# Optimization experiments

Hardware: AMD Instinct MI355X
Metric: run time of the kernel (lower is better)

The kernel has to match this reference:

```python
import jax, jax.numpy as jnp
import numpy as np

B, C, H, W = 8, 128, 64, 64


def setup_inputs() -> dict:
    key = jax.random.key(0)
    ks = jax.random.split(key, 8)
    s = 1.0 / np.sqrt(C)
    return {
        "x1": jax.random.normal(ks[0], (B, C, H, W), dtype=jnp.float32),
        "x2": jax.random.normal(ks[1], (B, C, H, W), dtype=jnp.float32),
        "Wq": jax.random.normal(ks[2], (C, C), dtype=jnp.float32) * s,
        "bq": jax.random.normal(ks[3], (C,), dtype=jnp.float32) * s,
        "Wk": jax.random.normal(ks[4], (C, C), dtype=jnp.float32) * s,
        "bk": jax.random.normal(ks[5], (C,), dtype=jnp.float32) * s,
        "Wv": jax.random.normal(ks[6], (C, C), dtype=jnp.float32) * s,
        "bv": jax.random.normal(ks[7], (C,), dtype=jnp.float32) * s,
    }


def reference(x1, x2, Wq, bq, Wk, bk, Wv, bv):
    b, c, h, w = x1.shape
    n = h * w
    # 1x1 conv == channel matmul per pixel; flatten spatial dims -> [b, c, n]
    x1f = x1.reshape(b, c, n)
    x2f = x2.reshape(b, c, n)
    q = jnp.einsum("oc,bcn->bno", Wq, x1f) + bq[None, None, :]  # [b, n, c]
    k = jnp.einsum("oc,bcn->bon", Wk, x2f) + bk[None, :, None]  # [b, c, n]
    v = jnp.einsum("oc,bcn->bon", Wv, x2f) + bv[None, :, None]  # [b, c, n]
    energy = jnp.einsum("bnc,bcm->bnm", q, k)                   # [b, n, n] (unscaled)
    attention = jax.nn.softmax(energy, axis=-1)
    # out[b,c,i] = sum_j v[b,c,j] * attention[b,i,j]
    out = jnp.einsum("bcj,bij->bci", v, attention)
    return out.reshape(b, c, h, w)
```

## Files before the change

kernel.cpp:

```cpp
#include <hip/hip_runtime.h>

typedef float f4 __attribute__((ext_vector_type(4)));
typedef float f16v __attribute__((ext_vector_type(16)));
typedef _Float16 hf;
typedef __fp16 fp16x2 __attribute__((ext_vector_type(2)));
typedef hf h8 __attribute__((ext_vector_type(8)));
typedef unsigned short ushort_t;
typedef unsigned int uint_t;
typedef uint_t u4 __attribute__((ext_vector_type(4)));

#define BATCH 8
#define CH 128
#define NPIX 4096
#define LOG2E 1.4426950408889634f
#define XSTR 65
#define RESCALE_THR 8.0f

__device__ inline f16v mfma32h(h8 a, h8 b, f16v c) {
    return __builtin_amdgcn_mfma_f32_32x32x16_f16(a, b, c, 0, 0, 0);
}

__device__ inline uint_t pk2h(float a, float b) {
    fp16x2 pp = __builtin_amdgcn_cvt_pkrtz(a, b);
    union { fp16x2 v; uint_t u; } cv;
    cv.v = pp;
    return cv.u;
}

__device__ inline void pl32swap(uint_t& a, uint_t& b) {
    asm("v_permlane32_swap_b32 %0, %1" : "+v"(a), "+v"(b));
}

typedef __attribute__((address_space(3))) uint_t lds_uint;
typedef __attribute__((address_space(1))) const uint_t global_uint;
__device__ inline void dma16(const void* g, void* l) {
    __builtin_amdgcn_global_load_lds((global_uint*)g, (lds_uint*)l, 16, 0, 0);
}

__global__ __launch_bounds__(256) void wprep_kernel(const float* __restrict__ Wq,
                                                    const float* __restrict__ Wk,
                                                    const float* __restrict__ Wv,
                                                    hf* __restrict__ WqT, hf* __restrict__ WkT,
                                                    hf* __restrict__ Wv16) {
    int m = blockIdx.x;
    const float* W = (m == 0) ? Wq : (m == 1) ? Wk : Wv;
    float s = (m == 0) ? LOG2E : 1.0f;
    for (int idx = threadIdx.x; idx < CH * CH; idx += 256) {
        int o = idx >> 7, c = idx & 127;
        float v = W[idx] * s;
        if (m == 0) WqT[c * CH + o] = (hf)v;
        else if (m == 1) WkT[c * CH + o] = (hf)v;
        else Wv16[idx] = (hf)v;
    }
}

__global__ __launch_bounds__(256) void qkv_kernel(const float* __restrict__ x1,
                                                  const float* __restrict__ x2,
                                                  const hf* __restrict__ WqT,
                                                  const hf* __restrict__ WkT,
                                                  const hf* __restrict__ Wv16,
                                                  const float* __restrict__ bq,
                                                  const float* __restrict__ bk,
                                                  const float* __restrict__ bv,
                                                  hf* __restrict__ Qf, hf* __restrict__ Kf,
                                                  hf* __restrict__ Vf) {
    __shared__ __align__(16) float Xs[CH * XSTR];

    int bid = blockIdx.x;
    int m = bid >> 9;
    int rem = bid & 511;
    int b = rem & 7;
    int n0 = (rem >> 3) << 6;

    const float* X = ((m == 0) ? x1 : x2) + (size_t)b * CH * NPIX;
    const float* bias = (m == 0) ? bq : (m == 1) ? bk : bv;

    int tid = threadIdx.x;
#pragma unroll
    for (int r = 0; r < 8; ++r) {
        int c = 16 * r + (tid >> 4);
        int n4 = (tid & 15) << 2;
        f4 v = *(const f4*)&X[(size_t)c * NPIX + n0 + n4];
#pragma unroll
        for (int j = 0; j < 4; ++j) Xs[c * XSTR + n4 + j] = v[j];
    }
    __syncthreads();

    int lane = tid & 63;
    int w = tid >> 6;
    int h = lane >> 5;
    int m32 = lane & 31;
    int o0 = w * 32;

    h8 wf[8];
    if (m == 2) {
#pragma unroll
        for (int kc = 0; kc < 8; ++kc)
            wf[kc] = *(const h8*)&Wv16[(size_t)(o0 + m32) * CH + kc * 16 + h * 8];
    } else {
        const hf* WT = (m == 0) ? WqT : WkT;
#pragma unroll
        for (int kc = 0; kc < 8; ++kc) {
            h8 t;
#pragma unroll
            for (int j = 0; j < 8; ++j) t[j] = WT[(size_t)(kc * 16 + h * 8 + j) * CH + o0 + m32];
            wf[kc] = t;
        }
    }

    f16v acc[2];
#pragma unroll
    for (int g = 0; g < 2; ++g)
#pragma unroll
        for (int r = 0; r < 16; ++r) acc[g][r] = 0.f;

#pragma unroll
    for (int g = 0; g < 2; ++g) {
        const float* xbase = &Xs[h * 8 * XSTR + g * 32 + m32];
#pragma unroll
        for (int kc = 0; kc < 8; ++kc) {
            h8 xh, xl;
#pragma unroll
            for (int j = 0; j < 8; ++j) {
                float f = xbase[(kc * 16 + j) * XSTR];
                hf hi = (hf)f;
                xh[j] = hi;
                xl[j] = (hf)(f - (float)hi);
            }
            if (m == 2) {
                acc[g] = mfma32h(wf[kc], xh, acc[g]);
                acc[g] = mfma32h(wf[kc], xl, acc[g]);
            } else {
                acc[g] = mfma32h(xh, wf[kc], acc[g]);
                acc[g] = mfma32h(xl, wf[kc], acc[g]);
            }
        }
    }

    if (m < 2) {
        float bval = bias[o0 + m32] * ((m == 0) ? LOG2E : 1.0f);
        hf* Y = ((m == 0) ? Qf : Kf) + (size_t)b * NPIX * CH;
#pragma unroll
        for (int g = 0; g < 2; ++g)
#pragma unroll
            for (int r = 0; r < 16; ++r) {
                int n = n0 + g * 32 + (r & 3) + 8 * (r >> 2) + 4 * h;
                Y[(size_t)n * CH + o0 + m32] = (hf)(acc[g][r] + bval);
            }
    } else {
        hf* Yv = Vf + (size_t)b * CH * NPIX;
#pragma unroll
        for (int g = 0; g < 2; ++g)
#pragma unroll
            for (int r = 0; r < 16; ++r) {
                int o = o0 + (r & 3) + 8 * (r >> 2) + 4 * h;
                Yv[(size_t)o * NPIX + n0 + g * 32 + m32] = (hf)(acc[g][r] + bias[o]);
            }
    }
}

__global__ __launch_bounds__(256, 2) void attn_kernel(const hf* __restrict__ Qf,
                                                      const hf* __restrict__ Kf,
                                                      const hf* __restrict__ Vf,
                                                      hf* __restrict__ Opart,
                                                      float* __restrict__ Mpart,
                                                      float* __restrict__ Lpart) {
    __shared__ __align__(16) ushort_t smem[32768];

    int tid = threadIdx.x;
    int lane = tid & 63;
    int w = tid >> 6;
    int h = lane >> 5;
    int m32 = lane & 31;
    int qh = w >> 1, kh = w & 1;

    int idx = blockIdx.x;
    int b = idx & 7;
    int ks = (idx >> 3) & 1;
    int qt = idx >> 4;
    int i0g = qt << 7;
    int k0g = ks << 11;
    int krow = kh * 32 + m32;

    const hf* Qb = Qf + (size_t)b * NPIX * CH;
    const hf* Kb = Kf + (size_t)b * NPIX * CH;
    const hf* Vb = Vf + (size_t)b * CH * NPIX;

    h8 qf[2][8];
#pragma unroll
    for (int g = 0; g < 2; ++g) {
        size_t row = (size_t)(i0g + qh * 64 + g * 32 + m32) * CH + h * 8;
#pragma unroll
        for (int kc = 0; kc < 8; ++kc) qf[g][kc] = *(const h8*)&Qb[row + kc * 16];
    }

    const hf* pK[4];
    const hf* pV[4];
#pragma unroll
    for (int a = 0; a < 4; ++a) {
        int g = w * 4 + a;
        int rowk = g * 4 + (lane >> 4);
        int lck = (lane & 15) ^ (rowk & 15);
        pK[a] = Kb + (size_t)(k0g + rowk) * CH + lck * 8;
        int rowv = g * 8 + (lane >> 3);
        int lcv = (lane & 7) ^ (rowv & 7);
        pV[a] = Vb + (size_t)rowv * NPIX + k0g + lcv * 8;
    }

#pragma unroll
    for (int a = 0; a < 4; ++a) {
        dma16(pK[a], &smem[(w * 4 + a) * 512]);
        dma16(pV[a], &smem[16384 + (w * 4 + a) * 512]);
        pK[a] += 64 * CH;
        pV[a] += 64;
    }

    f16v accO[2][4];
#pragma unroll
    for (int g = 0; g < 2; ++g)
#pragma unroll
        for (int ct = 0; ct < 4; ++ct)
#pragma unroll
            for (int r = 0; r < 16; ++r) accO[g][ct][r] = 0.f;
    float mprev[2] = {-1e30f, -1e30f};
    float lsum[2] = {0.f, 0.f};

    int pc2s[2];
#pragma unroll
    for (int g2 = 0; g2 < 2; ++g2) pc2s[g2] = (kh * 4 + g2 * 2 + h) ^ (m32 & 7);

    __syncthreads();

    for (int t = 0; t < 32; ++t) {
        int cur = t & 1;
        if (t < 31) {
            int nb = 1 - cur;
#pragma unroll
            for (int a = 0; a < 4; ++a) {
                dma16(pK[a], &smem[nb * 8192 + (w * 4 + a) * 512]);
                dma16(pV[a], &smem[16384 + nb * 8192 + (w * 4 + a) * 512]);
                pK[a] += 64 * CH;
                pV[a] += 64;
            }
        }
        const ushort_t* kb = smem + cur * 8192;
        const ushort_t* vb = smem + 16384 + cur * 8192;

        f16v acc0, acc1;
#pragma unroll
        for (int r = 0; r < 16; ++r) { acc0[r] = 0.f; acc1[r] = 0.f; }
        __builtin_amdgcn_s_setprio(1);
#pragma unroll
        for (int kc = 0; kc < 8; ++kc) {
            int pA = (kc * 2 + h) ^ (m32 & 15);
            h8 ahi = *(const h8*)&kb[krow * 128 + pA * 8];
            acc0 = mfma32h(ahi, qf[0][kc], acc0);
            acc1 = mfma32h(ahi, qf[1][kc], acc1);
        }
        __builtin_amdgcn_s_setprio(0);

        h8 pbp[2][2];
#pragma unroll
        for (int g = 0; g < 2; ++g) {
            f16v& acc = g ? acc1 : acc0;
            float ta = fmaxf(fmaxf(acc[0], acc[1]), acc[2]);
            float tb = fmaxf(fmaxf(acc[3], acc[4]), acc[5]);
            ta = fmaxf(fmaxf(ta, acc[6]), acc[7]);
            tb = fmaxf(fmaxf(tb, acc[8]), acc[9]);
            ta = fmaxf(fmaxf(ta, acc[10]), acc[11]);
            tb = fmaxf(fmaxf(tb, acc[12]), acc[13]);
            ta = fmaxf(fmaxf(ta, acc[14]), acc[15]);
            float tmax = fmaxf(ta, tb);
            tmax = fmaxf(tmax, __shfl_xor(tmax, 32));
            if (__any(tmax > mprev[g] + RESCALE_THR)) {
                float mnew = fmaxf(mprev[g], tmax);
                float alpha = exp2f(mprev[g] - mnew);
                lsum[g] *= alpha;
#pragma unroll
                for (int ct = 0; ct < 4; ++ct)
#pragma unroll
                    for (int r = 0; r < 16; ++r) accO[g][ct][r] *= alpha;
                mprev[g] = mnew;
            }

            float p[16];
#pragma unroll
            for (int r = 0; r < 16; ++r) p[r] = exp2f(acc[r] - mprev[g]);
            float ps[8];
#pragma unroll
            for (int r = 0; r < 8; ++r) ps[r] = p[r] + p[r + 8];
#pragma unroll
            for (int r = 0; r < 4; ++r) ps[r] += ps[r + 4];
            float psum = (ps[0] + ps[1]) + (ps[2] + ps[3]);
            psum += __shfl_xor(psum, 32);
            lsum[g] += psum;

            uint_t pk[8];
#pragma unroll
            for (int t2 = 0; t2 < 8; ++t2) pk[t2] = pk2h(p[2 * t2], p[2 * t2 + 1]);
            pl32swap(pk[0], pk[2]);
            pl32swap(pk[1], pk[3]);
            pl32swap(pk[4], pk[6]);
            pl32swap(pk[5], pk[7]);
#pragma unroll
            for (int g2 = 0; g2 < 2; ++g2) {
                u4 fv;
                fv[0] = pk[g2 * 4 + 0];
                fv[1] = pk[g2 * 4 + 1];
                fv[2] = pk[g2 * 4 + 2];
                fv[3] = pk[g2 * 4 + 3];
                __builtin_memcpy(&pbp[g][g2], &fv, 16);
            }
        }

        __builtin_amdgcn_s_setprio(1);
#pragma unroll
        for (int g2 = 0; g2 < 2; ++g2) {
            int pc2 = pc2s[g2];
#pragma unroll
            for (int ct = 0; ct < 4; ++ct) {
                h8 av = *(const h8*)&vb[(ct * 32 + m32) * 64 + pc2 * 8];
                accO[0][ct] = mfma32h(av, pbp[0][g2], accO[0][ct]);
                accO[1][ct] = mfma32h(av, pbp[1][g2], accO[1][ct]);
            }
        }
        __builtin_amdgcn_s_setprio(0);

        __syncthreads();
    }

    float* scr = (float*)smem;
    if (h == 0) {
#pragma unroll
        for (int g = 0; g < 2; ++g) {
            scr[kh * 128 + qh * 64 + g * 32 + m32] = mprev[g];
            scr[256 + kh * 128 + qh * 64 + g * 32 + m32] = lsum[g];
        }
    }
    __syncthreads();
    float fk[2], Mv[2], Lv[2];
#pragma unroll
    for (int g = 0; g < 2; ++g) {
        float mo = scr[(1 - kh) * 128 + qh * 64 + g * 32 + m32];
        float lo2 = scr[256 + (1 - kh) * 128 + qh * 64 + g * 32 + m32];
        float M = fmaxf(mprev[g], mo);
        fk[g] = exp2f(mprev[g] - M);
        float fo = exp2f(mo - M);
        Mv[g] = M;
        Lv[g] = lsum[g] * fk[g] + lo2 * fo;
    }
    __syncthreads();

    float* mrg = (float*)smem;
    if (kh == 1) {
#pragma unroll
        for (int g = 0; g < 2; ++g)
#pragma unroll
            for (int ct = 0; ct < 4; ++ct)
#pragma unroll
                for (int r = 0; r < 16; ++r) {
                    int ch = ct * 32 + (r & 3) + 8 * (r >> 2) + 4 * h;
                    mrg[ch * 128 + qh * 64 + g * 32 + m32] = accO[g][ct][r] * fk[g];
                }
    }
    __syncthreads();
    if (kh == 0) {
        size_t base = (((size_t)ks * 8 + b) * 32 + qt) * 16384;
        size_t mlb = (((size_t)ks * 8 + b) * 32 + qt) * 128;
#pragma unroll
        for (int g = 0; g < 2; ++g) {
            int q = qh * 64 + g * 32 + m32;
#pragma unroll
            for (int ct = 0; ct < 4; ++ct)
#pragma unroll
                for (int r = 0; r < 16; ++r) {
                    int ch = ct * 32 + (r & 3) + 8 * (r >> 2) + 4 * h;
                    Opart[base + ch * 128 + q] = (hf)(accO[g][ct][r] * fk[g] + mrg[ch * 128 + q]);
                }
            if (h == 0) {
                Mpart[mlb + q] = Mv[g];
                Lpart[mlb + q] = Lv[g];
            }
        }
    }
}

__global__ __launch_bounds__(256) void combine_kernel(const hf* __restrict__ Opart,
                                                      const float* __restrict__ Mp,
                                                      const float* __restrict__ Lp,
                                                      float* __restrict__ out) {
    int idx = blockIdx.x;
    int b = idx & 7;
    int qt = idx >> 3;
    int tid = threadIdx.x;
    int q = tid & 127;
    int ch0 = (tid >> 7) << 6;

    size_t base0 = (((size_t)b) * 32 + qt) * 16384;
    size_t base1 = ((((size_t)8 + b)) * 32 + qt) * 16384;
    size_t ml0 = (((size_t)b) * 32 + qt) * 128 + q;
    size_t ml1 = ((((size_t)8 + b)) * 32 + qt) * 128 + q;

    float M0 = Mp[ml0], M1 = Mp[ml1];
    float L0 = Lp[ml0], L1 = Lp[ml1];
    float M = fmaxf(M0, M1);
    float w0 = exp2f(M0 - M), w1 = exp2f(M1 - M);
    float rd = 1.0f / (w0 * L0 + w1 * L1);

    float* O = out + (size_t)b * CH * NPIX + ((size_t)qt << 7);
#pragma unroll 4
    for (int c = ch0; c < ch0 + 64; ++c) {
        float o0 = (float)Opart[base0 + c * 128 + q];
        float o1 = (float)Opart[base1 + c * 128 + q];
        O[(size_t)c * NPIX + q] = (w0 * o0 + w1 * o1) * rd;
    }
}

extern "C" void kernel_launch(void* const* d_in, const int* in_sizes, int n_in,
                              void* d_out, int out_size, void* d_ws, size_t ws_size,
                              hipStream_t stream) {
    const float* x1 = (const float*)d_in[0];
    const float* x2 = (const float*)d_in[1];
    const float* Wq = (const float*)d_in[2];
    const float* bq = (const float*)d_in[3];
    const float* Wk = (const float*)d_in[4];
    const float* bk = (const float*)d_in[5];
    const float* Wv = (const float*)d_in[6];
    const float* bv = (const float*)d_in[7];
    float* outp = (float*)d_out;

    const size_t N = (size_t)BATCH * NPIX * CH;
    hf* Qf = (hf*)d_ws;
    hf* Kf = Qf + N;
    hf* Vf = Qf + 2 * N;
    hf* WqT = Qf + 3 * N;
    hf* WkT = WqT + CH * CH;
    hf* Wv16 = WqT + 2 * CH * CH;
    hf* Opart = WqT + 3 * CH * CH;
    float* Mp = (float*)(Opart + (size_t)2 * 8 * 32 * 16384);
    float* Lp = Mp + (size_t)2 * 8 * 32 * 128;

    wprep_kernel<<<3, 256, 0, stream>>>(Wq, Wk, Wv, WqT, WkT, Wv16);
    qkv_kernel<<<3 * BATCH * (NPIX / 64), 256, 0, stream>>>(x1, x2, WqT, WkT, Wv16,
                                                            bq, bk, bv, Qf, Kf, Vf);
    attn_kernel<<<BATCH * 2 * (NPIX / 128), 256, 0, stream>>>(Qf, Kf, Vf, Opart, Mp, Lp);
    combine_kernel<<<BATCH * (NPIX / 128), 256, 0, stream>>>(Opart, Mp, Lp, outp);
}
```

Before: 237.1 us.

## Split attention into four key chunks with one query tile per wave

The attention kernel changes from two key splits with a 2x2 wave grid (query half by key half, merged inside the block through LDS) to four key splits where each wave owns 32 queries and walks all keys of its chunk. This drops the in-block merge, halves LDS so three blocks fit per CU, and doubles the grid. The cost is twice the partial-output traffic, handled by a combine kernel that now merges four partials with vectorized loads and stores. The separate weight-prep kernel is also removed: the QKV kernel reads the fp32 weights directly and converts them, saving one launch.

```diff
diff --git a/kernel.cpp b/kernel.cpp
--- a/kernel.cpp
+++ b/kernel.cpp
@@ -37,28 +37,11 @@
     __builtin_amdgcn_global_load_lds((global_uint*)g, (lds_uint*)l, 16, 0, 0);
 }
 
-__global__ __launch_bounds__(256) void wprep_kernel(const float* __restrict__ Wq,
-                                                    const float* __restrict__ Wk,
-                                                    const float* __restrict__ Wv,
-                                                    hf* __restrict__ WqT, hf* __restrict__ WkT,
-                                                    hf* __restrict__ Wv16) {
-    int m = blockIdx.x;
-    const float* W = (m == 0) ? Wq : (m == 1) ? Wk : Wv;
-    float s = (m == 0) ? LOG2E : 1.0f;
-    for (int idx = threadIdx.x; idx < CH * CH; idx += 256) {
-        int o = idx >> 7, c = idx & 127;
-        float v = W[idx] * s;
-        if (m == 0) WqT[c * CH + o] = (hf)v;
-        else if (m == 1) WkT[c * CH + o] = (hf)v;
-        else Wv16[idx] = (hf)v;
-    }
-}
-
 __global__ __launch_bounds__(256) void qkv_kernel(const float* __restrict__ x1,
                                                   const float* __restrict__ x2,
-                                                  const hf* __restrict__ WqT,
-                                                  const hf* __restrict__ WkT,
-                                                  const hf* __restrict__ Wv16,
+                                                  const float* __restrict__ Wq,
+                                                  const float* __restrict__ Wk,
+                                                  const float* __restrict__ Wv,
                                                   const float* __restrict__ bq,
                                                   const float* __restrict__ bk,
                                                   const float* __restrict__ bv,
@@ -92,18 +75,21 @@
     int m32 = lane & 31;
     int o0 = w * 32;
 
+    const float* Wsrc = (m == 0) ? Wq : (m == 1) ? Wk : Wv;
+    float wscale = (m == 0) ? LOG2E : 1.0f;
     h8 wf[8];
-    if (m == 2) {
-#pragma unroll
-        for (int kc = 0; kc < 8; ++kc)
-            wf[kc] = *(const h8*)&Wv16[(size_t)(o0 + m32) * CH + kc * 16 + h * 8];
-    } else {
-        const hf* WT = (m == 0) ? WqT : WkT;
+    {
+        const float* wrow = Wsrc + (size_t)(o0 + m32) * CH;
 #pragma unroll
         for (int kc = 0; kc < 8; ++kc) {
+            f4 a = *(const f4*)&wrow[kc * 16 + h * 8];
+            f4 b2 = *(const f4*)&wrow[kc * 16 + h * 8 + 4];
             h8 t;
 #pragma unroll
-            for (int j = 0; j < 8; ++j) t[j] = WT[(size_t)(kc * 16 + h * 8 + j) * CH + o0 + m32];
+            for (int j = 0; j < 4; ++j) {
+                t[j] = (hf)(a[j] * wscale);
+                t[4 + j] = (hf)(b2[j] * wscale);
+            }
             wf[kc] = t;
         }
     }
@@ -159,75 +145,68 @@
     }
 }
 
-__global__ __launch_bounds__(256, 2) void attn_kernel(const hf* __restrict__ Qf,
+__global__ __launch_bounds__(256, 3) void attn_kernel(const hf* __restrict__ Qf,
                                                       const hf* __restrict__ Kf,
                                                       const hf* __restrict__ Vf,
                                                       hf* __restrict__ Opart,
                                                       float* __restrict__ Mpart,
                                                       float* __restrict__ Lpart) {
-    __shared__ __align__(16) ushort_t smem[32768];
+    __shared__ __align__(16) ushort_t smem[16384];
 
     int tid = threadIdx.x;
     int lane = tid & 63;
     int w = tid >> 6;
     int h = lane >> 5;
     int m32 = lane & 31;
-    int qh = w >> 1, kh = w & 1;
 
     int idx = blockIdx.x;
     int b = idx & 7;
-    int ks = (idx >> 3) & 1;
-    int qt = idx >> 4;
-    int i0g = qt << 7;
-    int k0g = ks << 11;
-    int krow = kh * 32 + m32;
+    int ks = (idx >> 3) & 3;
+    int qt = idx >> 5;
+    int q0 = (qt << 7) + w * 32;
+    int k0g = ks << 10;
 
     const hf* Qb = Qf + (size_t)b * NPIX * CH;
     const hf* Kb = Kf + (size_t)b * NPIX * CH;
     const hf* Vb = Vf + (size_t)b * CH * NPIX;
 
-    h8 qf[2][8];
-#pragma unroll
-    for (int g = 0; g < 2; ++g) {
-        size_t row = (size_t)(i0g + qh * 64 + g * 32 + m32) * CH + h * 8;
-#pragma unroll
-        for (int kc = 0; kc < 8; ++kc) qf[g][kc] = *(const h8*)&Qb[row + kc * 16];
-    }
-
-    const hf* pK[4];
-    const hf* pV[4];
-#pragma unroll
-    for (int a = 0; a < 4; ++a) {
-        int g = w * 4 + a;
-        int rowk = g * 4 + (lane >> 4);
+    h8 qf[8];
+#pragma unroll
+    for (int kc = 0; kc < 8; ++kc)
+        qf[kc] = *(const h8*)&Qb[(size_t)(q0 + m32) * CH + kc * 16 + h * 8];
+
+    const hf* pK[2];
+    const hf* pV[2];
+#pragma unroll
+    for (int a = 0; a < 2; ++a) {
+        int chunk_hi = w * 2 + a;
+        int rowk = chunk_hi * 4 + (lane >> 4);
         int lck = (lane & 15) ^ (rowk & 15);
         pK[a] = Kb + (size_t)(k0g + rowk) * CH + lck * 8;
-        int rowv = g * 8 + (lane >> 3);
-        int lcv = (lane & 7) ^ (rowv & 7);
+        int rowv = chunk_hi * 16 + (lane >> 2);
+        int lcv = (lane & 3) ^ (rowv & 3);
         pV[a] = Vb + (size_t)rowv * NPIX + k0g + lcv * 8;
     }
 
 #pragma unroll
-    for (int a = 0; a < 4; ++a) {
-        dma16(pK[a], &smem[(w * 4 + a) * 512]);
-        dma16(pV[a], &smem[16384 + (w * 4 + a) * 512]);
-        pK[a] += 64 * CH;
-        pV[a] += 64;
-    }
-
-    f16v accO[2][4];
-#pragma unroll
-    for (int g = 0; g < 2; ++g)
-#pragma unroll
-        for (int ct = 0; ct < 4; ++ct)
-#pragma unroll
-            for (int r = 0; r < 16; ++r) accO[g][ct][r] = 0.f;
-    float mprev[2] = {-1e30f, -1e30f};
-    float lsum[2] = {0.f, 0.f};
-
-    int pc2s[2];
-#pragma unroll
-    for (int g2 = 0; g2 < 2; ++g2) pc2s[g2] = (kh * 4 + g2 * 2 + h) ^ (m32 & 7);
+    for (int a = 0; a < 2; ++a) {
+        dma16(pK[a], &smem[(w * 2 + a) * 512]);
+        dma16(pV[a], &smem[8192 + (w * 2 + a) * 512]);
+        pK[a] += 32 * CH;
+        pV[a] += 32;
+    }
+
+    f16v accO[4];
+#pragma unroll
+    for (int ct = 0; ct < 4; ++ct)
+#pragma unroll
+        for (int r = 0; r < 16; ++r) accO[ct][r] = 0.f;
+    float mprev = -1e30f;
+    float lsum = 0.f;
+
+    int pvs[2];
+#pragma unroll
+    for (int g2 = 0; g2 < 2; ++g2) pvs[g2] = (g2 * 2 + h) ^ (m32 & 3);
 
     __syncthreads();
 
@@ -236,92 +215,85 @@
         if (t < 31) {
             int nb = 1 - cur;
 #pragma unroll
-            for (int a = 0; a < 4; ++a) {
-                dma16(pK[a], &smem[nb * 8192 + (w * 4 + a) * 512]);
-                dma16(pV[a], &smem[16384 + nb * 8192 + (w * 4 + a) * 512]);
-                pK[a] += 64 * CH;
-                pV[a] += 64;
-            }
-        }
-        const ushort_t* kb = smem + cur * 8192;
-        const ushort_t* vb = smem + 16384 + cur * 8192;
-
-        f16v acc0, acc1;
-#pragma unroll
-        for (int r = 0; r < 16; ++r) { acc0[r] = 0.f; acc1[r] = 0.f; }
+            for (int a = 0; a < 2; ++a) {
+                dma16(pK[a], &smem[nb * 4096 + (w * 2 + a) * 512]);
+                dma16(pV[a], &smem[8192 + nb * 4096 + (w * 2 + a) * 512]);
+                pK[a] += 32 * CH;
+                pV[a] += 32;
+            }
+        }
+        const ushort_t* kb = smem + cur * 4096;
+        const ushort_t* vb = smem + 8192 + cur * 4096;
+
+        f16v acc;
+#pragma unroll
+        for (int r = 0; r < 16; ++r) acc[r] = 0.f;
         __builtin_amdgcn_s_setprio(1);
 #pragma unroll
         for (int kc = 0; kc < 8; ++kc) {
             int pA = (kc * 2 + h) ^ (m32 & 15);
-            h8 ahi = *(const h8*)&kb[krow * 128 + pA * 8];
-            acc0 = mfma32h(ahi, qf[0][kc], acc0);
-            acc1 = mfma32h(ahi, qf[1][kc], acc1);
+            h8 ahi = *(const h8*)&kb[m32 * 128 + pA * 8];
+            acc = mfma32h(ahi, qf[kc], acc);
         }
         __builtin_amdgcn_s_setprio(0);
 
-        h8 pbp[2][2];
-#pragma unroll
-        for (int g = 0; g < 2; ++g) {
-            f16v& acc = g ? acc1 : acc0;
-            float ta = fmaxf(fmaxf(acc[0], acc[1]), acc[2]);
-            float tb = fmaxf(fmaxf(acc[3], acc[4]), acc[5]);
-            ta = fmaxf(fmaxf(ta, acc[6]), acc[7]);
-            tb = fmaxf(fmaxf(tb, acc[8]), acc[9]);
-            ta = fmaxf(fmaxf(ta, acc[10]), acc[11]);
-            tb = fmaxf(fmaxf(tb, acc[12]), acc[13]);
-            ta = fmaxf(fmaxf(ta, acc[14]), acc[15]);
-            float tmax = fmaxf(ta, tb);
-            tmax = fmaxf(tmax, __shfl_xor(tmax, 32));
-            if (__any(tmax > mprev[g] + RESCALE_THR)) {
-                float mnew = fmaxf(mprev[g], tmax);
-                float alpha = exp2f(mprev[g] - mnew);
-                lsum[g] *= alpha;
-#pragma unroll
-                for (int ct = 0; ct < 4; ++ct)
-#pragma unroll
-                    for (int r = 0; r < 16; ++r) accO[g][ct][r] *= alpha;
-                mprev[g] = mnew;
-            }
-
-            float p[16];
-#pragma unroll
-            for (int r = 0; r < 16; ++r) p[r] = exp2f(acc[r] - mprev[g]);
-            float ps[8];
-#pragma unroll
-            for (int r = 0; r < 8; ++r) ps[r] = p[r] + p[r + 8];
-#pragma unroll
-            for (int r = 0; r < 4; ++r) ps[r] += ps[r + 4];
-            float psum = (ps[0] + ps[1]) + (ps[2] + ps[3]);
-            psum += __shfl_xor(psum, 32);
-            lsum[g] += psum;
-
-            uint_t pk[8];
-#pragma unroll
-            for (int t2 = 0; t2 < 8; ++t2) pk[t2] = pk2h(p[2 * t2], p[2 * t2 + 1]);
-            pl32swap(pk[0], pk[2]);
-            pl32swap(pk[1], pk[3]);
-            pl32swap(pk[4], pk[6]);
-            pl32swap(pk[5], pk[7]);
-#pragma unroll
-            for (int g2 = 0; g2 < 2; ++g2) {
-                u4 fv;
-                fv[0] = pk[g2 * 4 + 0];
-                fv[1] = pk[g2 * 4 + 1];
-                fv[2] = pk[g2 * 4 + 2];
-                fv[3] = pk[g2 * 4 + 3];
-                __builtin_memcpy(&pbp[g][g2], &fv, 16);
-            }
+        float ta = fmaxf(fmaxf(acc[0], acc[1]), acc[2]);
+        float tb = fmaxf(fmaxf(acc[3], acc[4]), acc[5]);
+        ta = fmaxf(fmaxf(ta, acc[6]), acc[7]);
+        tb = fmaxf(fmaxf(tb, acc[8]), acc[9]);
+        ta = fmaxf(fmaxf(ta, acc[10]), acc[11]);
+        tb = fmaxf(fmaxf(tb, acc[12]), acc[13]);
+        ta = fmaxf(fmaxf(ta, acc[14]), acc[15]);
+        float tmax = fmaxf(ta, tb);
+        tmax = fmaxf(tmax, __shfl_xor(tmax, 32));
+        if (__any(tmax > mprev + RESCALE_THR)) {
+            float mnew = fmaxf(mprev, tmax);
+            float alpha = exp2f(mprev - mnew);
+            lsum *= alpha;
+#pragma unroll
+            for (int ct = 0; ct < 4; ++ct)
+#pragma unroll
+                for (int r = 0; r < 16; ++r) accO[ct][r] *= alpha;
+            mprev = mnew;
+        }
+
+        uint_t pk[8];
+        float ps0 = 0.f, ps1 = 0.f;
+#pragma unroll
+        for (int t2 = 0; t2 < 8; ++t2) {
+            float e0 = exp2f(acc[2 * t2] - mprev);
+            float e1 = exp2f(acc[2 * t2 + 1] - mprev);
+            ps0 += e0;
+            ps1 += e1;
+            pk[t2] = pk2h(e0, e1);
+        }
+        float psum = ps0 + ps1;
+        psum += __shfl_xor(psum, 32);
+        lsum += psum;
+
+        pl32swap(pk[0], pk[2]);
+        pl32swap(pk[1], pk[3]);
+        pl32swap(pk[4], pk[6]);
+        pl32swap(pk[5], pk[7]);
+        h8 pbp[2];
+#pragma unroll
+        for (int g2 = 0; g2 < 2; ++g2) {
+            u4 fv;
+            fv[0] = pk[g2 * 4 + 0];
+            fv[1] = pk[g2 * 4 + 1];
+            fv[2] = pk[g2 * 4 + 2];
+            fv[3] = pk[g2 * 4 + 3];
+            __builtin_memcpy(&pbp[g2], &fv, 16);
         }
 
         __builtin_amdgcn_s_setprio(1);
 #pragma unroll
         for (int g2 = 0; g2 < 2; ++g2) {
-            int pc2 = pc2s[g2];
+            int pv = pvs[g2];
 #pragma unroll
             for (int ct = 0; ct < 4; ++ct) {
-                h8 av = *(const h8*)&vb[(ct * 32 + m32) * 64 + pc2 * 8];
-                accO[0][ct] = mfma32h(av, pbp[0][g2], accO[0][ct]);
-                accO[1][ct] = mfma32h(av, pbp[1][g2], accO[1][ct]);
+                h8 av = *(const h8*)&vb[(ct * 32 + m32) * 32 + pv * 8];
+                accO[ct] = mfma32h(av, pbp[g2], accO[ct]);
             }
         }
         __builtin_amdgcn_s_setprio(0);
@@ -329,59 +301,19 @@
         __syncthreads();
     }
 
-    float* scr = (float*)smem;
+    size_t base = (((size_t)ks * 8 + b) * 32 + qt) * 16384;
+    size_t mlb = (((size_t)ks * 8 + b) * 32 + qt) * 128;
+    int q = w * 32 + m32;
+#pragma unroll
+    for (int ct = 0; ct < 4; ++ct)
+#pragma unroll
+        for (int r = 0; r < 16; ++r) {
+            int ch = ct * 32 + (r & 3) + 8 * (r >> 2) + 4 * h;
+            Opart[base + ch * 128 + q] = (hf)accO[ct][r];
+        }
     if (h == 0) {
-#pragma unroll
-        for (int g = 0; g < 2; ++g) {
-            scr[kh * 128 + qh * 64 + g * 32 + m32] = mprev[g];
-            scr[256 + kh * 128 + qh * 64 + g * 32 + m32] = lsum[g];
-        }
-    }
-    __syncthreads();
-    float fk[2], Mv[2], Lv[2];
-#pragma unroll
-    for (int g = 0; g < 2; ++g) {
-        float mo = scr[(1 - kh) * 128 + qh * 64 + g * 32 + m32];
-        float lo2 = scr[256 + (1 - kh) * 128 + qh * 64 + g * 32 + m32];
-        float M = fmaxf(mprev[g], mo);
-        fk[g] = exp2f(mprev[g] - M);
-        float fo = exp2f(mo - M);
-        Mv[g] = M;
-        Lv[g] = lsum[g] * fk[g] + lo2 * fo;
-    }
-    __syncthreads();
-
-    float* mrg = (float*)smem;
-    if (kh == 1) {
-#pragma unroll
-        for (int g = 0; g < 2; ++g)
-#pragma unroll
-            for (int ct = 0; ct < 4; ++ct)
-#pragma unroll
-                for (int r = 0; r < 16; ++r) {
-                    int ch = ct * 32 + (r & 3) + 8 * (r >> 2) + 4 * h;
-                    mrg[ch * 128 + qh * 64 + g * 32 + m32] = accO[g][ct][r] * fk[g];
-                }
-    }
-    __syncthreads();
-    if (kh == 0) {
-        size_t base = (((size_t)ks * 8 + b) * 32 + qt) * 16384;
-        size_t mlb = (((size_t)ks * 8 + b) * 32 + qt) * 128;
-#pragma unroll
-        for (int g = 0; g < 2; ++g) {
-            int q = qh * 64 + g * 32 + m32;
-#pragma unroll
-            for (int ct = 0; ct < 4; ++ct)
-#pragma unroll
-                for (int r = 0; r < 16; ++r) {
-                    int ch = ct * 32 + (r & 3) + 8 * (r >> 2) + 4 * h;
-                    Opart[base + ch * 128 + q] = (hf)(accO[g][ct][r] * fk[g] + mrg[ch * 128 + q]);
-                }
-            if (h == 0) {
-                Mpart[mlb + q] = Mv[g];
-                Lpart[mlb + q] = Lv[g];
-            }
-        }
+        Mpart[mlb + q] = mprev;
+        Lpart[mlb + q] = lsum;
     }
 }
 
@@ -390,29 +322,72 @@
                                                       const float* __restrict__ Lp,
                                                       float* __restrict__ out) {
     int idx = blockIdx.x;
-    int b = idx & 7;
-    int qt = idx >> 3;
+    int chh = idx & 1;
+    int b = (idx >> 1) & 7;
+    int qt = idx >> 4;
     int tid = threadIdx.x;
-    int q = tid & 127;
-    int ch0 = (tid >> 7) << 6;
-
-    size_t base0 = (((size_t)b) * 32 + qt) * 16384;
-    size_t base1 = ((((size_t)8 + b)) * 32 + qt) * 16384;
-    size_t ml0 = (((size_t)b) * 32 + qt) * 128 + q;
-    size_t ml1 = ((((size_t)8 + b)) * 32 + qt) * 128 + q;
-
-    float M0 = Mp[ml0], M1 = Mp[ml1];
-    float L0 = Lp[ml0], L1 = Lp[ml1];
-    float M = fmaxf(M0, M1);
-    float w0 = exp2f(M0 - M), w1 = exp2f(M1 - M);
-    float rd = 1.0f / (w0 * L0 + w1 * L1);
-
-    float* O = out + (size_t)b * CH * NPIX + ((size_t)qt << 7);
-#pragma unroll 4
-    for (int c = ch0; c < ch0 + 64; ++c) {
-        float o0 = (float)Opart[base0 + c * 128 + q];
-        float o1 = (float)Opart[base1 + c * 128 + q];
-        O[(size_t)c * NPIX + q] = (w0 * o0 + w1 * o1) * rd;
+    int q8 = (tid & 15) << 3;
+    int chl = tid >> 4;
+
+    size_t tile = (size_t)b * 32 + qt;
+
+    float Marr[4][8], Larr[4][8];
+#pragma unroll
+    for (int p = 0; p < 4; ++p) {
+        const float* mp_ = Mp + ((size_t)p * 256 + tile) * 128 + q8;
+        const float* lp_ = Lp + ((size_t)p * 256 + tile) * 128 + q8;
+        f4 ma = *(const f4*)mp_;
+        f4 mb = *(const f4*)(mp_ + 4);
+        f4 la = *(const f4*)lp_;
+        f4 lb = *(const f4*)(lp_ + 4);
+#pragma unroll
+        for (int j = 0; j < 4; ++j) {
+            Marr[p][j] = ma[j];
+            Marr[p][4 + j] = mb[j];
+            Larr[p][j] = la[j];
+            Larr[p][4 + j] = lb[j];
+        }
+    }
+
+    float wgt[4][8];
+#pragma unroll
+    for (int j = 0; j < 8; ++j) {
+        float M = fmaxf(fmaxf(Marr[0][j], Marr[1][j]), fmaxf(Marr[2][j], Marr[3][j]));
+        float L = 0.f;
+#pragma unroll
+        for (int p = 0; p < 4; ++p) {
+            float w_ = exp2f(Marr[p][j] - M);
+            wgt[p][j] = w_;
+            L += w_ * Larr[p][j];
+        }
+        float rd = 1.0f / L;
+#pragma unroll
+        for (int p = 0; p < 4; ++p) wgt[p][j] *= rd;
+    }
+
+    const hf* ob[4];
+#pragma unroll
+    for (int p = 0; p < 4; ++p) ob[p] = Opart + ((size_t)p * 256 + tile) * 16384 + q8;
+    float* O = out + (size_t)b * CH * NPIX + (size_t)qt * 128 + q8;
+
+#pragma unroll
+    for (int it = 0; it < 4; ++it) {
+        int ch = chh * 64 + it * 16 + chl;
+        union { u4 u; h8 v; } o4[4];
+#pragma unroll
+        for (int p = 0; p < 4; ++p) o4[p].u = *(const u4*)&ob[p][(size_t)ch * 128];
+        f4 r0, r1;
+#pragma unroll
+        for (int j = 0; j < 8; ++j) {
+            float s = 0.f;
+#pragma unroll
+            for (int p = 0; p < 4; ++p) s += wgt[p][j] * (float)o4[p].v[j];
+            if (j < 4) r0[j] = s;
+            else r1[j - 4] = s;
+        }
+        float* dst = O + (size_t)ch * NPIX;
+        *(f4*)dst = r0;
+        *(f4*)(dst + 4) = r1;
     }
 }
 
@@ -433,16 +408,12 @@
     hf* Qf = (hf*)d_ws;
     hf* Kf = Qf + N;
     hf* Vf = Qf + 2 * N;
-    hf* WqT = Qf + 3 * N;
-    hf* WkT = WqT + CH * CH;
-    hf* Wv16 = WqT + 2 * CH * CH;
-    hf* Opart = WqT + 3 * CH * CH;
-    float* Mp = (float*)(Opart + (size_t)2 * 8 * 32 * 16384);
-    float* Lp = Mp + (size_t)2 * 8 * 32 * 128;
-
-    wprep_kernel<<<3, 256, 0, stream>>>(Wq, Wk, Wv, WqT, WkT, Wv16);
-    qkv_kernel<<<3 * BATCH * (NPIX / 64), 256, 0, stream>>>(x1, x2, WqT, WkT, Wv16,
+    hf* Opart = Qf + 3 * N;
+    float* Mp = (float*)(Opart + (size_t)4 * 8 * 32 * 16384);
+    float* Lp = Mp + (size_t)4 * 8 * 32 * 128;
+
+    qkv_kernel<<<3 * BATCH * (NPIX / 64), 256, 0, stream>>>(x1, x2, Wq, Wk, Wv,
                                                             bq, bk, bv, Qf, Kf, Vf);
-    attn_kernel<<<BATCH * 2 * (NPIX / 128), 256, 0, stream>>>(Qf, Kf, Vf, Opart, Mp, Lp);
-    combine_kernel<<<BATCH * (NPIX / 128), 256, 0, stream>>>(Opart, Mp, Lp, outp);
-}
+    attn_kernel<<<BATCH * 4 * (NPIX / 128), 256, 0, stream>>>(Qf, Kf, Vf, Opart, Mp, Lp);
+    combine_kernel<<<2 * BATCH * (NPIX / 128), 256, 0, stream>>>(Opart, Mp, Lp, outp);
+}
```

Result: faster. 214.8 us (-9.4%).
